# Kernel optimization log

Hardware: AMD Instinct MI355X
Metric: run time of the kernel (lower is better)

The kernel has to match this reference:

```python
import jax, jax.numpy as jnp
import numpy as np

N = 20000      # total nodes
E = 320000     # edges before self loops
G = 64         # graphs in the batch
H = 8          # attention heads
NEG_SLOPE = 0.2
EPS = 1e-5


def _gatv2(x, src, dst, Wl, bl, Wr, br, att, bias, concat):
    # PyG GATv2Conv: xl = lin_l(x) (source/messages), xr = lin_r(x) (target)
    heads, C = att.shape
    xl = (x @ Wl + bl).reshape(-1, heads, C)
    xr = (x @ Wr + br).reshape(-1, heads, C)
    e = jax.nn.leaky_relu(xl[src] + xr[dst], NEG_SLOPE)          # [E', H, C]
    a = jnp.einsum('ehc,hc->eh', e, att)                          # [E', H]
    amax = jax.ops.segment_max(a, dst, num_segments=N)
    a = jnp.exp(a - amax[dst])
    a = a / jax.ops.segment_sum(a, dst, num_segments=N)[dst]
    out = jax.ops.segment_sum(xl[src] * a[..., None], dst, num_segments=N)
    out = out.reshape(-1, heads * C) if concat else out.mean(axis=1)
    return out + bias


def _graphnorm(x, batch, w, b, ms):
    cnt = jnp.maximum(jax.ops.segment_sum(jnp.ones((x.shape[0],), x.dtype), batch, num_segments=G), 1.0)[:, None]
    mean = jax.ops.segment_sum(x, batch, num_segments=G) / cnt
    out = x - mean[batch] * ms
    var = jax.ops.segment_sum(out * out, batch, num_segments=G) / cnt
    return w * out / jnp.sqrt(var + EPS)[batch] + b


def _mean_pool(x, batch):
    cnt = jnp.maximum(jax.ops.segment_sum(jnp.ones((x.shape[0],), x.dtype), batch, num_segments=G), 1.0)[:, None]
    return jax.ops.segment_sum(x, batch, num_segments=G) / cnt


def setup_inputs():
    key = jax.random.key(0)
    ks = iter(jax.random.split(key, 40))

    def gl(shape, scale=0.05):
        return jax.random.normal(next(ks), shape, jnp.float32) * scale

    inp = {}
    inp['x'] = jax.random.normal(next(ks), (N, 19), jnp.float32)
    inp['edge_index'] = jax.random.randint(next(ks), (2, E), 0, N, jnp.int32)
    inp['batch'] = jnp.sort(jax.random.randint(next(ks), (N,), 0, G, jnp.int32))

    # layer 1: 19 -> (8 heads x 32), concat -> 256
    inp['W1l'] = gl((19, 256)); inp['b1l'] = jnp.zeros((256,), jnp.float32)
    inp['W1r'] = gl((19, 256)); inp['b1r'] = jnp.zeros((256,), jnp.float32)
    inp['att1'] = gl((H, 32)); inp['bias1'] = jnp.zeros((256,), jnp.float32)
    inp['gn1_w'] = jnp.ones((256,), jnp.float32); inp['gn1_b'] = jnp.zeros((256,), jnp.float32); inp['gn1_ms'] = jnp.ones((256,), jnp.float32)

    inp['W2l'] = gl((256, 128)); inp['b2l'] = jnp.zeros((128,), jnp.float32)
    inp['W2r'] = gl((256, 128)); inp['b2r'] = jnp.zeros((128,), jnp.float32)
    inp['att2'] = gl((H, 16)); inp['bias2'] = jnp.zeros((128,), jnp.float32)
    inp['gn2_w'] = jnp.ones((128,), jnp.float32); inp['gn2_b'] = jnp.zeros((128,), jnp.float32); inp['gn2_ms'] = jnp.ones((128,), jnp.float32)

    inp['W3l'] = gl((128, 64)); inp['b3l'] = jnp.zeros((64,), jnp.float32)
    inp['W3r'] = gl((128, 64)); inp['b3r'] = jnp.zeros((64,), jnp.float32)
    inp['att3'] = gl((H, 8)); inp['bias3'] = jnp.zeros((8,), jnp.float32)
    inp['gn3_w'] = jnp.ones((8,), jnp.float32); inp['gn3_b'] = jnp.zeros((8,), jnp.float32); inp['gn3_ms'] = jnp.ones((8,), jnp.float32)

    inp['lin_w'] = gl((8, 4)); inp['lin_b'] = jnp.zeros((4,), jnp.float32)
    return inp


def reference(x, edge_index, batch, W1l, b1l, W1r, b1r, att1, bias1, gn1_w, gn1_b, gn1_ms,
              W2l, b2l, W2r, b2r, att2, bias2, gn2_w, gn2_b, gn2_ms,
              W3l, b3l, W3r, b3r, att3, bias3, gn3_w, gn3_b, gn3_ms, lin_w, lin_b):
    loop = jnp.arange(N, dtype=edge_index.dtype)  # GATv2Conv add_self_loops=True
    src = jnp.concatenate([edge_index[0], loop])
    dst = jnp.concatenate([edge_index[1], loop])

    h = _gatv2(x, src, dst, W1l, b1l, W1r, b1r, att1, bias1, True)
    h = jax.nn.relu(_graphnorm(h, batch, gn1_w, gn1_b, gn1_ms))
    h = _gatv2(h, src, dst, W2l, b2l, W2r, b2r, att2, bias2, True)
    h = jax.nn.relu(_graphnorm(h, batch, gn2_w, gn2_b, gn2_ms))
    h = _gatv2(h, src, dst, W3l, b3l, W3r, b3r, att3, bias3, False)
    h = jax.nn.relu(_graphnorm(h, batch, gn3_w, gn3_b, gn3_ms))

    features = _mean_pool(h, batch)        # [G, 8]
    logits = features @ lin_w + lin_b      # [G, 4]
    return (logits, features)
```

## Files before the change

kernel.cpp:

```cpp
#include <hip/hip_runtime.h>
#include <math.h>

#define NN 20000
#define EE 320000
#define GG 64
#define HH 8
#define EPSV 1e-5f

static inline unsigned int gridFor(long n, int b){ return (unsigned int)((n + b - 1)/b); }

typedef __attribute__((ext_vector_type(8))) short short8;
typedef __attribute__((ext_vector_type(4))) float f32x4;
typedef unsigned short ushort_t;

__device__ __forceinline__ float asf(unsigned int u){
    union{unsigned int i; float f;} c; c.i = u; return c.f;
}
__device__ __forceinline__ ushort_t f2bf(float x){
    unsigned u = __float_as_uint(x);
    unsigned r = u + 0x7FFFu + ((u >> 16) & 1u);
    return (ushort_t)(r >> 16);
}
__device__ __forceinline__ void split_bf16(float x, short& hi, short& lo){
    unsigned u = __float_as_uint(x);
    unsigned r = u + 0x7FFFu + ((u >> 16) & 1u);
    hi = (short)(r >> 16);
    float hf = asf(((unsigned)(unsigned short)hi) << 16);
    float res = x - hf;
    unsigned u2 = __float_as_uint(res);
    unsigned r2 = u2 + 0x7FFFu + ((u2 >> 16) & 1u);
    lo = (short)(r2 >> 16);
}

__device__ __forceinline__ void wprep_one(const float* Wl, const float* Wr,
                                          ushort_t* Whi, ushort_t* Wlo,
                                          int K, int Kp, int HC, int t){
    int octs = Kp >> 3;
    int n = t / octs, ko = t - n*octs;
    int kb = ko*8;
    const float* W = (n < HC) ? (Wl + n) : (Wr + (n - HC));
    short hi[8], lo[8];
    #pragma unroll
    for (int j = 0; j < 8; ++j){
        int k = kb + j;
        float v = (k < K) ? W[(long)k*HC] : 0.f;
        split_bf16(v, hi[j], lo[j]);
    }
    long base = (((long)(n>>4)*(Kp>>5) + (kb>>5))*64 + (n&15) + 16*((kb>>3)&3))*8;
    *(short8*)&Whi[base] = *(short8*)hi;
    *(short8*)&Wlo[base] = *(short8*)lo;
}

#define WP1 2048
#define WP2 8192
#define WP3 2048

__global__ void k_wprep_all(const float* __restrict__ W1l, const float* __restrict__ W1r,
                            const float* __restrict__ W2l, const float* __restrict__ W2r,
                            const float* __restrict__ W3l, const float* __restrict__ W3r,
                            ushort_t* __restrict__ W1hi, ushort_t* __restrict__ W1lo,
                            ushort_t* __restrict__ W2hi, ushort_t* __restrict__ W2lo,
                            ushort_t* __restrict__ W3hi, ushort_t* __restrict__ W3lo,
                            int* __restrict__ cursor){
    int t = blockIdx.x*blockDim.x + threadIdx.x;
    if (t < NN) cursor[t] = 0;
    if (t < WP1) wprep_one(W1l, W1r, W1hi, W1lo, 19, 32, 256, t);
    else if (t < WP1+WP2) wprep_one(W2l, W2r, W2hi, W2lo, 256, 256, 128, t-WP1);
    else if (t < WP1+WP2+WP3) wprep_one(W3l, W3r, W3hi, W3lo, 128, 128, 64, t-WP1-WP2);
}

__global__ void k_degbounds(const int* __restrict__ edst, int* __restrict__ deg,
                            const int* __restrict__ batch,
                            int* __restrict__ gstart, int* __restrict__ gend,
                            float* __restrict__ gz){
    int e = blockIdx.x*blockDim.x + threadIdx.x;
    if (e < EE) atomicAdd(&deg[edst[e]], 1);
    if (e < NN){
        int b = batch[e];
        if (e == 0 || batch[e-1] != b) gstart[b] = e;
        if (e == NN-1 || batch[e+1] != b) gend[b] = e+1;
    }
    if (e < 2*GG*256) gz[e] = 0.f;
}

__global__ void k_scan(int* __restrict__ deg, int* __restrict__ indptr){
    __shared__ int partial[1024];
    const int CH = (NN + 1023)/1024;
    int t = threadIdx.x;
    int base = t*CH;
    int vals[CH];
    int sum = 0;
    for (int i = 0; i < CH; ++i){
        int v = (base+i < NN) ? deg[base+i] : 0;
        vals[i] = sum; sum += v;
    }
    for (int i = 0; i < CH; ++i)
        if (base+i < NN) deg[base+i] = 0;
    partial[t] = sum;
    __syncthreads();
    for (int off = 1; off < 1024; off <<= 1){
        int v = (t >= off) ? partial[t-off] : 0;
        __syncthreads();
        partial[t] += v;
        __syncthreads();
    }
    int prefix = (t > 0) ? partial[t-1] : 0;
    for (int i = 0; i < CH; ++i)
        if (base+i < NN) indptr[base+i] = prefix + vals[i];
    if (t == 1023) indptr[NN] = prefix + sum;
}

__global__ void k_scatter(const int* __restrict__ esrc, const int* __restrict__ edst,
                          const int* __restrict__ indptr, int* __restrict__ cursor,
                          int* __restrict__ srclist){
    int e = blockIdx.x*blockDim.x + threadIdx.x;
    if (e >= EE) return;
    int d = edst[e];
    int pos = atomicAdd(&cursor[d], 1);
    srclist[indptr[d] + pos] = esrc[e];
}

template<bool NORM>
__global__ __launch_bounds__(256)
void k_gemm_mfma(const float* __restrict__ h,
                 const ushort_t* __restrict__ Whi, const ushort_t* __restrict__ Wlo,
                 const float* __restrict__ bl, const float* __restrict__ br,
                 const float* __restrict__ gmu, const float* __restrict__ ginv,
                 const float* __restrict__ nw, const float* __restrict__ nb,
                 const int* __restrict__ batch,
                 ushort_t* __restrict__ xlb, float* __restrict__ xr,
                 int K, int Kp, int HC){
    __shared__ short Ahi[2][64*32], Alo[2][64*32];
    const int tid  = threadIdx.x;
    const int lane = tid & 63;
    const int wave = tid >> 6;
    const int m0   = blockIdx.x * 64;
    const int n0   = blockIdx.y * 128;
    const int wr   = (wave & 1) * 32;
    const int wcg  = (wave >> 1) * 64;
    const int kblocks = Kp >> 5;

    const int srow = tid >> 2;
    const int soct = tid & 3;

    f32x4 acc[2][4] = {};

    for (int kb = 0; kb < kblocks; ++kb){
        int p = kb & 1;
        int k0 = kb*32;
        {
            int gm = m0 + srow;
            int kbase = k0 + soct*8;
            float v[8];
            const float* src = h + (long)gm*K + kbase;
            if (gm < NN && kbase + 8 <= K){
                float4 t0 = *(const float4*)src;
                float4 t1 = *(const float4*)(src+4);
                v[0]=t0.x; v[1]=t0.y; v[2]=t0.z; v[3]=t0.w;
                v[4]=t1.x; v[5]=t1.y; v[6]=t1.z; v[7]=t1.w;
            } else {
                #pragma unroll
                for (int j = 0; j < 8; ++j)
                    v[j] = (gm < NN && kbase + j < K) ? src[j] : 0.f;
            }
            if (NORM && gm < NN){
                int g = batch[gm];
                const float* mu = gmu + (long)g*K;
                const float* iv = ginv + (long)g*K;
                #pragma unroll
                for (int j = 0; j < 8; ++j){
                    int c = kbase + j;
                    float t = (v[j] - mu[c]) * iv[c] * nw[c] + nb[c];
                    v[j] = fmaxf(t, 0.f);
                }
            }
            short hi[8], lo[8];
            #pragma unroll
            for (int j = 0; j < 8; ++j) split_bf16(v[j], hi[j], lo[j]);
            long off = ((long)(srow>>4)*64 + (srow&15) + 16*soct)*8;
            *(short8*)&Ahi[p][off] = *(short8*)hi;
            *(short8*)&Alo[p][off] = *(short8*)lo;
        }
        __syncthreads();

        int rb0 = wr >> 4;
        short8 ah0 = *(short8*)&Ahi[p][((rb0  )*64 + lane)*8];
        short8 ah1 = *(short8*)&Ahi[p][((rb0+1)*64 + lane)*8];
        short8 al0 = *(short8*)&Alo[p][((rb0  )*64 + lane)*8];
        short8 al1 = *(short8*)&Alo[p][((rb0+1)*64 + lane)*8];

        short8 bh[4], bl_[4];
        #pragma unroll
        for (int j = 0; j < 4; ++j){
            int n = n0 + wcg + j*16;
            long bbase = (((long)(n>>4)*kblocks + kb)*64 + lane)*8;
            bh[j]  = *(const short8*)&Whi[bbase];
            bl_[j] = *(const short8*)&Wlo[bbase];
        }

        #pragma unroll
        for (int j = 0; j < 4; ++j){
            acc[0][j] = __builtin_amdgcn_mfma_f32_16x16x32_bf16(al0, bh[j],  acc[0][j], 0,0,0);
            acc[0][j] = __builtin_amdgcn_mfma_f32_16x16x32_bf16(ah0, bl_[j], acc[0][j], 0,0,0);
            acc[0][j] = __builtin_amdgcn_mfma_f32_16x16x32_bf16(ah0, bh[j],  acc[0][j], 0,0,0);
            acc[1][j] = __builtin_amdgcn_mfma_f32_16x16x32_bf16(al1, bh[j],  acc[1][j], 0,0,0);
            acc[1][j] = __builtin_amdgcn_mfma_f32_16x16x32_bf16(ah1, bl_[j], acc[1][j], 0,0,0);
            acc[1][j] = __builtin_amdgcn_mfma_f32_16x16x32_bf16(ah1, bh[j],  acc[1][j], 0,0,0);
        }
    }

    #pragma unroll
    for (int i = 0; i < 2; ++i){
        int row0 = m0 + wr + i*16 + (lane >> 4)*4;
        #pragma unroll
        for (int j = 0; j < 4; ++j){
            int n = n0 + wcg + j*16 + (lane & 15);
            float bb = (n < HC) ? bl[n] : br[n - HC];
            #pragma unroll
            for (int r = 0; r < 4; ++r){
                int gm = row0 + r;
                if (gm >= NN) continue;
                float v = acc[i][j][r] + bb;
                if (n < HC) xlb[(long)gm*HC + n] = f2bf(v);
                else        xr[(long)gm*HC + (n - HC)] = v;
            }
        }
    }
}

template<int VEC> struct VT;
template<> struct VT<1>{ using T = float;  };
template<> struct VT<2>{ using T = float2; };
template<> struct VT<4>{ using T = float4; };

template<int VEC> struct BF;
template<> struct BF<1>{
    static __device__ __forceinline__ float load(const ushort_t* p){
        return asf(((unsigned)*p) << 16);
    }
};
template<> struct BF<2>{
    static __device__ __forceinline__ float2 load(const ushort_t* p){
        unsigned u = *(const unsigned*)p;
        return make_float2(asf(u << 16), asf(u & 0xFFFF0000u));
    }
};
template<> struct BF<4>{
    static __device__ __forceinline__ float4 load(const ushort_t* p){
        uint2 u = *(const uint2*)p;
        return make_float4(asf(u.x << 16), asf(u.x & 0xFFFF0000u),
                           asf(u.y << 16), asf(u.y & 0xFFFF0000u));
    }
};

__device__ __forceinline__ float lrelu(float z){ return z > 0.f ? z : 0.2f*z; }

__device__ __forceinline__ float edot(float xv, float xr, float at){
    return lrelu(xv + xr) * at;
}
__device__ __forceinline__ float edot(float2 xv, float2 xr, float2 at){
    return lrelu(xv.x+xr.x)*at.x + lrelu(xv.y+xr.y)*at.y;
}
__device__ __forceinline__ float edot(float4 xv, float4 xr, float4 at){
    return lrelu(xv.x+xr.x)*at.x + lrelu(xv.y+xr.y)*at.y
         + lrelu(xv.z+xr.z)*at.z + lrelu(xv.w+xr.w)*at.w;
}
__device__ __forceinline__ void efma(float& o, float p, float xv){ o = fmaf(p,xv,o); }
__device__ __forceinline__ void efma(float2& o, float p, float2 xv){
    o.x = fmaf(p,xv.x,o.x); o.y = fmaf(p,xv.y,o.y);
}
__device__ __forceinline__ void efma(float4& o, float p, float4 xv){
    o.x = fmaf(p,xv.x,o.x); o.y = fmaf(p,xv.y,o.y);
    o.z = fmaf(p,xv.z,o.z); o.w = fmaf(p,xv.w,o.w);
}
__device__ __forceinline__ float escale(float o, float s, float b){ return fmaf(o,s,b); }
__device__ __forceinline__ float2 escale(float2 o, float s, float2 b){
    return make_float2(fmaf(o.x,s,b.x), fmaf(o.y,s,b.y));
}
__device__ __forceinline__ float4 escale(float4 o, float s, float4 b){
    return make_float4(fmaf(o.x,s,b.x), fmaf(o.y,s,b.y), fmaf(o.z,s,b.z), fmaf(o.w,s,b.w));
}

__device__ __forceinline__ float red8(float v){
    v += __shfl_xor(v, 1);
    v += __shfl_xor(v, 2);
    v += __shfl_xor(v, 4);
    return v;
}

template<int VEC, bool MEAN>
__global__ __launch_bounds__(256)
void k_gat_w(const int* __restrict__ indptr, const int* __restrict__ srclist,
             const ushort_t* __restrict__ xlb, const float* __restrict__ xr,
             const float* __restrict__ att, const float* __restrict__ bias,
             float* __restrict__ val){
    using V = typename VT<VEC>::T;
    constexpr int HC = 64*VEC;
    const int lane = threadIdx.x & 63;
    const int d = blockIdx.x*4 + (threadIdx.x >> 6);
    const int co = lane*VEC;

    V xrd = *(const V*)&xr[(long)d*HC + co];
    V at  = *(const V*)&att[co];
    V xls = BF<VEC>::load(xlb + (long)d*HC + co);

    float m0 = red8(edot(xls, xrd, at));
    float l = 1.0f;
    V o = xls;

    int j = indptr[d], end = indptr[d+1];
    for (; j + 8 <= end; j += 8){
        int s0 = srclist[j+0], s1 = srclist[j+1], s2 = srclist[j+2], s3 = srclist[j+3];
        int s4 = srclist[j+4], s5 = srclist[j+5], s6 = srclist[j+6], s7 = srclist[j+7];
        V x0 = BF<VEC>::load(xlb + (long)s0*HC + co);
        V x1 = BF<VEC>::load(xlb + (long)s1*HC + co);
        V x2 = BF<VEC>::load(xlb + (long)s2*HC + co);
        V x3 = BF<VEC>::load(xlb + (long)s3*HC + co);
        V x4 = BF<VEC>::load(xlb + (long)s4*HC + co);
        V x5 = BF<VEC>::load(xlb + (long)s5*HC + co);
        V x6 = BF<VEC>::load(xlb + (long)s6*HC + co);
        V x7 = BF<VEC>::load(xlb + (long)s7*HC + co);
        float a0 = red8(edot(x0, xrd, at));
        float a1 = red8(edot(x1, xrd, at));
        float a2 = red8(edot(x2, xrd, at));
        float a3 = red8(edot(x3, xrd, at));
        float a4 = red8(edot(x4, xrd, at));
        float a5 = red8(edot(x5, xrd, at));
        float a6 = red8(edot(x6, xrd, at));
        float a7 = red8(edot(x7, xrd, at));
        float p0 = __expf(a0 - m0), p1 = __expf(a1 - m0);
        float p2 = __expf(a2 - m0), p3 = __expf(a3 - m0);
        float p4 = __expf(a4 - m0), p5 = __expf(a5 - m0);
        float p6 = __expf(a6 - m0), p7 = __expf(a7 - m0);
        l += ((p0+p1)+(p2+p3)) + ((p4+p5)+(p6+p7));
        efma(o, p0, x0); efma(o, p1, x1); efma(o, p2, x2); efma(o, p3, x3);
        efma(o, p4, x4); efma(o, p5, x5); efma(o, p6, x6); efma(o, p7, x7);
    }
    for (; j < end; j += 4){
        int m = end - j;
        int s0 = srclist[j];
        int s1 = (m > 1) ? srclist[j+1] : s0;
        int s2 = (m > 2) ? srclist[j+2] : s0;
        int s3 = (m > 3) ? srclist[j+3] : s0;
        V x0 = BF<VEC>::load(xlb + (long)s0*HC + co);
        V x1 = BF<VEC>::load(xlb + (long)s1*HC + co);
        V x2 = BF<VEC>::load(xlb + (long)s2*HC + co);
        V x3 = BF<VEC>::load(xlb + (long)s3*HC + co);
        float a0 = red8(edot(x0, xrd, at));
        float a1 = red8(edot(x1, xrd, at));
        float a2 = red8(edot(x2, xrd, at));
        float a3 = red8(edot(x3, xrd, at));
        float p0 = __expf(a0 - m0);
        float p1 = __expf(a1 - m0);
        float p2 = __expf(a2 - m0);
        float p3 = __expf(a3 - m0);
        l += p0; efma(o, p0, x0);
        if (m > 1){ l += p1; efma(o, p1, x1); }
        if (m > 2){ l += p2; efma(o, p2, x2); }
        if (m > 3){ l += p3; efma(o, p3, x3); }
    }
    float invl = 1.0f / l;
    if (!MEAN){
        V bv = *(const V*)&bias[co];
        *(V*)&val[(long)d*HC + co] = escale(o, invl, bv);
    } else {
        float r = ((float&)o) * invl;
        r += __shfl_xor(r, 8);
        r += __shfl_xor(r, 16);
        r += __shfl_xor(r, 32);
        if (lane < 8) val[(long)d*8 + lane] = r*0.125f + bias[lane];
    }
}

template<int F>
__global__ void k_gn_partial(const float* __restrict__ val,
                             const int* __restrict__ gstart, const int* __restrict__ gend,
                             float* __restrict__ gsum, float* __restrict__ gsq){
    int g = blockIdx.x, ch = blockIdx.y, nch = gridDim.y;
    int c = threadIdx.x;
    int s = gstart[g], e = gend[g];
    float sum = 0.f, sq = 0.f;
    for (int i = s + ch; i < e; i += nch){
        float v = val[(long)i*F + c];
        sum += v; sq += v*v;
    }
    if (sum != 0.f || sq != 0.f){
        atomicAdd(&gsum[g*F + c], sum);
        atomicAdd(&gsq[g*F + c], sq);
    }
}

__global__ void k_gn_finalize(float* __restrict__ gsum, float* __restrict__ gsq,
                              const int* __restrict__ gstart, const int* __restrict__ gend,
                              const float* __restrict__ ms,
                              float* __restrict__ gmu, float* __restrict__ ginv, int F){
    int idx = blockIdx.x*blockDim.x + threadIdx.x;
    if (idx >= GG*F) return;
    int g = idx / F, c = idx - g*F;
    int cnti = gend[g] - gstart[g];
    float cn = cnti > 0 ? (float)cnti : 1.f;
    float mean = gsum[idx] / cn;
    float mu = mean * ms[c];
    float var = gsq[idx]/cn - 2.f*mu*mean + mu*mu;
    gmu[idx]  = mu;
    ginv[idx] = rsqrtf(var + EPSV);
    gsum[idx] = 0.f;
    gsq[idx]  = 0.f;
}

__global__ void k_tail(const float* __restrict__ D,
                       const int* __restrict__ gstart, const int* __restrict__ gend,
                       const float* __restrict__ ms, const float* __restrict__ w,
                       const float* __restrict__ b,
                       const float* __restrict__ lw, const float* __restrict__ lb,
                       float* __restrict__ outLog, float* __restrict__ outFeat){
    int g = blockIdx.x;
    int t = threadIdx.x;
    int c = t & 7, r = t >> 3;
    int s = gstart[g], e = gend[g];
    int cnti = e - s;
    float cn = cnti > 0 ? (float)cnti : 1.f;

    float sum = 0.f, sq = 0.f;
    for (int i = s + r; i < e; i += 8){
        float v = D[(long)i*8 + c];
        sum += v; sq += v*v;
    }
    #pragma unroll
    for (int mask = 8; mask < 64; mask <<= 1){
        sum += __shfl_xor(sum, mask, 64);
        sq  += __shfl_xor(sq,  mask, 64);
    }
    float mean = sum / cn;
    float mu = mean * ms[c];
    float var = sq/cn - 2.f*mu*mean + mu*mu;
    float iv = rsqrtf(var + EPSV);
    float wc = w[c], bc = b[c];

    float psum = 0.f;
    for (int i = s + r; i < e; i += 8){
        float v = (D[(long)i*8 + c] - mu) * iv * wc + bc;
        psum += fmaxf(v, 0.f);
    }
    #pragma unroll
    for (int mask = 8; mask < 64; mask <<= 1)
        psum += __shfl_xor(psum, mask, 64);
    float feat = psum / cn;

    if (t < 8) outFeat[g*8 + t] = feat;

    float a = 0.f;
    int jj = t;
    if (t < 4){
        a = lb[jj];
    }
    #pragma unroll
    for (int cc = 0; cc < 8; ++cc){
        float fc = __shfl(feat, cc, 64);
        if (t < 4) a += fc * lw[cc*4 + jj];
    }
    if (t < 4) outLog[g*4 + jj] = a;
}

extern "C" void kernel_launch(void* const* d_in, const int* in_sizes, int n_in,
                              void* d_out, int out_size, void* d_ws, size_t ws_size,
                              hipStream_t stream) {
    const float* x     = (const float*)d_in[0];
    const int*   ei    = (const int*)  d_in[1];
    const int*   batch = (const int*)  d_in[2];
    const float* W1l = (const float*)d_in[3];  const float* b1l = (const float*)d_in[4];
    const float* W1r = (const float*)d_in[5];  const float* b1r = (const float*)d_in[6];
    const float* att1= (const float*)d_in[7];  const float* bias1=(const float*)d_in[8];
    const float* g1w = (const float*)d_in[9];  const float* g1b = (const float*)d_in[10];
    const float* g1m = (const float*)d_in[11];
    const float* W2l = (const float*)d_in[12]; const float* b2l = (const float*)d_in[13];
    const float* W2r = (const float*)d_in[14]; const float* b2r = (const float*)d_in[15];
    const float* att2= (const float*)d_in[16]; const float* bias2=(const float*)d_in[17];
    const float* g2w = (const float*)d_in[18]; const float* g2b = (const float*)d_in[19];
    const float* g2m = (const float*)d_in[20];
    const float* W3l = (const float*)d_in[21]; const float* b3l = (const float*)d_in[22];
    const float* W3r = (const float*)d_in[23]; const float* b3r = (const float*)d_in[24];
    const float* att3= (const float*)d_in[25]; const float* bias3=(const float*)d_in[26];
    const float* g3w = (const float*)d_in[27]; const float* g3b = (const float*)d_in[28];
    const float* g3m = (const float*)d_in[29];
    const float* lin_w=(const float*)d_in[30]; const float* lin_b=(const float*)d_in[31];

    const int* esrc = ei;
    const int* edst = ei + EE;

    float* ws = (float*)d_ws;
    int*   cursor  = (int*)(ws + 0);
    int*   indptr  = (int*)(ws + 20480);
    int*   srclist = (int*)(ws + 40960);
    int*   gstart  = (int*)(ws + 361472);
    int*   gend    = (int*)(ws + 361984);
    float* gmu     = ws + 362496;
    float* ginv    = ws + 378880;
    float* gsumP   = ws + 395264;
    float* gsqP    = ws + 411648;
    ushort_t* W1hi = (ushort_t*)(ws + 428032);
    ushort_t* W1lo = (ushort_t*)(ws + 436224);
    ushort_t* W2hi = (ushort_t*)(ws + 444416);
    ushort_t* W2lo = (ushort_t*)(ws + 477184);
    ushort_t* W3hi = (ushort_t*)(ws + 509952);
    ushort_t* W3lo = (ushort_t*)(ws + 518144);
    ushort_t* Bb = (ushort_t*)(ws + 526336);
    float* Cb = ws + 3086336;
    float* D  = ws + 8206336;

    const int TB = 256;
    const int MBm = (NN + 63)/64;
    const int NCH = 32;

    k_wprep_all<<<gridFor(NN, TB), TB, 0, stream>>>(W1l, W1r, W2l, W2r, W3l, W3r,
        W1hi, W1lo, W2hi, W2lo, W3hi, W3lo, cursor);
    k_degbounds<<<gridFor(EE, TB), TB, 0, stream>>>(edst, cursor, batch, gstart, gend, gsumP);
    k_scan<<<1, 1024, 0, stream>>>(cursor, indptr);
    k_scatter<<<gridFor(EE, TB), TB, 0, stream>>>(esrc, edst, indptr, cursor, srclist);

    k_gemm_mfma<false><<<dim3(MBm, 4), 256, 0, stream>>>(x, W1hi, W1lo, b1l, b1r,
        nullptr, nullptr, nullptr, nullptr, nullptr, Bb, Cb, 19, 32, 256);
    k_gat_w<4, false><<<NN/4, 256, 0, stream>>>(indptr, srclist, Bb, Cb, att1, bias1, D);
    k_gn_partial<256><<<dim3(GG, NCH), 256, 0, stream>>>(D, gstart, gend, gsumP, gsqP);
    k_gn_finalize<<<gridFor(GG*256, TB), TB, 0, stream>>>(gsumP, gsqP, gstart, gend, g1m, gmu, ginv, 256);

    k_gemm_mfma<true><<<dim3(MBm, 2), 256, 0, stream>>>(D, W2hi, W2lo, b2l, b2r,
        gmu, ginv, g1w, g1b, batch, Bb, Cb, 256, 256, 128);
    k_gat_w<2, false><<<NN/4, 256, 0, stream>>>(indptr, srclist, Bb, Cb, att2, bias2, D);
    k_gn_partial<128><<<dim3(GG, NCH), 128, 0, stream>>>(D, gstart, gend, gsumP, gsqP);
    k_gn_finalize<<<gridFor(GG*128, TB), TB, 0, stream>>>(gsumP, gsqP, gstart, gend, g2m, gmu, ginv, 128);

    k_gemm_mfma<true><<<dim3(MBm, 1), 256, 0, stream>>>(D, W3hi, W3lo, b3l, b3r,
        gmu, ginv, g2w, g2b, batch, Bb, Cb, 128, 128, 64);
    k_gat_w<1, true><<<NN/4, 256, 0, stream>>>(indptr, srclist, Bb, Cb, att3, bias3, D);

    float* outLog  = (float*)d_out;
    float* outFeat = outLog + GG*4;
    k_tail<<<GG, 64, 0, stream>>>(D, gstart, gend, g3m, g3w, g3b, lin_w, lin_b, outLog, outFeat);
}
```

Measured before the change: 344.7 us.

## Split GAT aggregation across channel blocks, fuse scatter with first GEMM, vectorize scan

The layer-1 and layer-2 attention aggregation kernels now use one scalar channel per lane and split the channels over a second grid dimension. This gives more waves per destination node and uses narrower per-lane loads, but each slice re-reads the neighbour list. The edge-scatter CSR build is merged into the first GEMM launch as extra blocks, which removes one launch and lets the two run concurrently. The scan kernel loads and stores in int4 chunks, relying on NN being 1000*20.

```diff
diff --git a/kernel.cpp b/kernel.cpp
--- a/kernel.cpp
+++ b/kernel.cpp
@@ -85,17 +85,22 @@
 
 __global__ void k_scan(int* __restrict__ deg, int* __restrict__ indptr){
     __shared__ int partial[1024];
-    const int CH = (NN + 1023)/1024;
     int t = threadIdx.x;
-    int base = t*CH;
-    int vals[CH];
+    int vals[20];
     int sum = 0;
-    for (int i = 0; i < CH; ++i){
-        int v = (base+i < NN) ? deg[base+i] : 0;
-        vals[i] = sum; sum += v;
-    }
-    for (int i = 0; i < CH; ++i)
-        if (base+i < NN) deg[base+i] = 0;
+    if (t < 1000){
+        int4 buf[5];
+        const int4* p = (const int4*)(deg + t*20);
+        #pragma unroll
+        for (int i = 0; i < 5; ++i) buf[i] = p[i];
+        const int* bv = (const int*)buf;
+        #pragma unroll
+        for (int i = 0; i < 20; ++i){ vals[i] = sum; sum += bv[i]; }
+        int4 z = make_int4(0,0,0,0);
+        int4* pz = (int4*)(deg + t*20);
+        #pragma unroll
+        for (int i = 0; i < 5; ++i) pz[i] = z;
+    }
     partial[t] = sum;
     __syncthreads();
     for (int off = 1; off < 1024; off <<= 1){
@@ -105,37 +110,33 @@
         __syncthreads();
     }
     int prefix = (t > 0) ? partial[t-1] : 0;
-    for (int i = 0; i < CH; ++i)
-        if (base+i < NN) indptr[base+i] = prefix + vals[i];
-    if (t == 1023) indptr[NN] = prefix + sum;
-}
-
-__global__ void k_scatter(const int* __restrict__ esrc, const int* __restrict__ edst,
-                          const int* __restrict__ indptr, int* __restrict__ cursor,
-                          int* __restrict__ srclist){
-    int e = blockIdx.x*blockDim.x + threadIdx.x;
-    if (e >= EE) return;
-    int d = edst[e];
-    int pos = atomicAdd(&cursor[d], 1);
-    srclist[indptr[d] + pos] = esrc[e];
+    if (t < 1000){
+        int out[20];
+        #pragma unroll
+        for (int i = 0; i < 20; ++i) out[i] = prefix + vals[i];
+        int4* q = (int4*)(indptr + t*20);
+        #pragma unroll
+        for (int i = 0; i < 5; ++i) q[i] = ((const int4*)out)[i];
+    }
+    if (t == 1023) indptr[NN] = prefix;
 }
 
 template<bool NORM>
-__global__ __launch_bounds__(256)
-void k_gemm_mfma(const float* __restrict__ h,
-                 const ushort_t* __restrict__ Whi, const ushort_t* __restrict__ Wlo,
-                 const float* __restrict__ bl, const float* __restrict__ br,
-                 const float* __restrict__ gmu, const float* __restrict__ ginv,
-                 const float* __restrict__ nw, const float* __restrict__ nb,
-                 const int* __restrict__ batch,
-                 ushort_t* __restrict__ xlb, float* __restrict__ xr,
-                 int K, int Kp, int HC){
+__device__ __forceinline__ void gemm_body(
+    const float* __restrict__ h,
+    const ushort_t* __restrict__ Whi, const ushort_t* __restrict__ Wlo,
+    const float* __restrict__ bl, const float* __restrict__ br,
+    const float* __restrict__ gmu, const float* __restrict__ ginv,
+    const float* __restrict__ nw, const float* __restrict__ nb,
+    const int* __restrict__ batch,
+    ushort_t* __restrict__ xlb, float* __restrict__ xr,
+    int K, int Kp, int HC, int bm, int bn){
     __shared__ short Ahi[2][64*32], Alo[2][64*32];
     const int tid  = threadIdx.x;
     const int lane = tid & 63;
     const int wave = tid >> 6;
-    const int m0   = blockIdx.x * 64;
-    const int n0   = blockIdx.y * 128;
+    const int m0   = bm * 64;
+    const int n0   = bn * 128;
     const int wr   = (wave & 1) * 32;
     const int wcg  = (wave >> 1) * 64;
     const int kblocks = Kp >> 5;
@@ -228,113 +229,97 @@
     }
 }
 
-template<int VEC> struct VT;
-template<> struct VT<1>{ using T = float;  };
-template<> struct VT<2>{ using T = float2; };
-template<> struct VT<4>{ using T = float4; };
-
-template<int VEC> struct BF;
-template<> struct BF<1>{
-    static __device__ __forceinline__ float load(const ushort_t* p){
-        return asf(((unsigned)*p) << 16);
-    }
-};
-template<> struct BF<2>{
-    static __device__ __forceinline__ float2 load(const ushort_t* p){
-        unsigned u = *(const unsigned*)p;
-        return make_float2(asf(u << 16), asf(u & 0xFFFF0000u));
-    }
-};
-template<> struct BF<4>{
-    static __device__ __forceinline__ float4 load(const ushort_t* p){
-        uint2 u = *(const uint2*)p;
-        return make_float4(asf(u.x << 16), asf(u.x & 0xFFFF0000u),
-                           asf(u.y << 16), asf(u.y & 0xFFFF0000u));
-    }
-};
+template<bool NORM>
+__global__ __launch_bounds__(256)
+void k_gemm_mfma(const float* __restrict__ h,
+                 const ushort_t* __restrict__ Whi, const ushort_t* __restrict__ Wlo,
+                 const float* __restrict__ bl, const float* __restrict__ br,
+                 const float* __restrict__ gmu, const float* __restrict__ ginv,
+                 const float* __restrict__ nw, const float* __restrict__ nb,
+                 const int* __restrict__ batch,
+                 ushort_t* __restrict__ xlb, float* __restrict__ xr,
+                 int K, int Kp, int HC){
+    gemm_body<NORM>(h, Whi, Wlo, bl, br, gmu, ginv, nw, nb, batch, xlb, xr,
+                    K, Kp, HC, blockIdx.x, blockIdx.y);
+}
+
+__global__ __launch_bounds__(256)
+void k_gemm1_scatter(const float* __restrict__ x,
+                     const ushort_t* __restrict__ Whi, const ushort_t* __restrict__ Wlo,
+                     const float* __restrict__ bl, const float* __restrict__ br,
+                     ushort_t* __restrict__ xlb, float* __restrict__ xr,
+                     const int* __restrict__ esrc, const int* __restrict__ edst,
+                     const int* __restrict__ indptr, int* __restrict__ cursor,
+                     int* __restrict__ srclist, int nGemm, int mb){
+    if ((int)blockIdx.x < nGemm){
+        gemm_body<false>(x, Whi, Wlo, bl, br, nullptr, nullptr, nullptr, nullptr,
+                         nullptr, xlb, xr, 19, 32, 256, blockIdx.x % mb, blockIdx.x / mb);
+    } else {
+        int e = (blockIdx.x - nGemm)*256 + threadIdx.x;
+        if (e < EE){
+            int d = edst[e];
+            int pos = atomicAdd(&cursor[d], 1);
+            srclist[indptr[d] + pos] = esrc[e];
+        }
+    }
+}
 
 __device__ __forceinline__ float lrelu(float z){ return z > 0.f ? z : 0.2f*z; }
 
-__device__ __forceinline__ float edot(float xv, float xr, float at){
-    return lrelu(xv + xr) * at;
-}
-__device__ __forceinline__ float edot(float2 xv, float2 xr, float2 at){
-    return lrelu(xv.x+xr.x)*at.x + lrelu(xv.y+xr.y)*at.y;
-}
-__device__ __forceinline__ float edot(float4 xv, float4 xr, float4 at){
-    return lrelu(xv.x+xr.x)*at.x + lrelu(xv.y+xr.y)*at.y
-         + lrelu(xv.z+xr.z)*at.z + lrelu(xv.w+xr.w)*at.w;
-}
-__device__ __forceinline__ void efma(float& o, float p, float xv){ o = fmaf(p,xv,o); }
-__device__ __forceinline__ void efma(float2& o, float p, float2 xv){
-    o.x = fmaf(p,xv.x,o.x); o.y = fmaf(p,xv.y,o.y);
-}
-__device__ __forceinline__ void efma(float4& o, float p, float4 xv){
-    o.x = fmaf(p,xv.x,o.x); o.y = fmaf(p,xv.y,o.y);
-    o.z = fmaf(p,xv.z,o.z); o.w = fmaf(p,xv.w,o.w);
-}
-__device__ __forceinline__ float escale(float o, float s, float b){ return fmaf(o,s,b); }
-__device__ __forceinline__ float2 escale(float2 o, float s, float2 b){
-    return make_float2(fmaf(o.x,s,b.x), fmaf(o.y,s,b.y));
-}
-__device__ __forceinline__ float4 escale(float4 o, float s, float4 b){
-    return make_float4(fmaf(o.x,s,b.x), fmaf(o.y,s,b.y), fmaf(o.z,s,b.z), fmaf(o.w,s,b.w));
-}
-
-__device__ __forceinline__ float red8(float v){
-    v += __shfl_xor(v, 1);
-    v += __shfl_xor(v, 2);
-    v += __shfl_xor(v, 4);
+template<int C>
+__device__ __forceinline__ float redC(float v){
+    #pragma unroll
+    for (int m = 1; m < C; m <<= 1) v += __shfl_xor(v, m);
     return v;
 }
-
-template<int VEC, bool MEAN>
+__device__ __forceinline__ float bfld(const ushort_t* p){
+    return asf(((unsigned)*p) << 16);
+}
+
+template<int C>
 __global__ __launch_bounds__(256)
-void k_gat_w(const int* __restrict__ indptr, const int* __restrict__ srclist,
+void k_gat_s(const int* __restrict__ indptr, const int* __restrict__ srclist,
              const ushort_t* __restrict__ xlb, const float* __restrict__ xr,
              const float* __restrict__ att, const float* __restrict__ bias,
-             float* __restrict__ val){
-    using V = typename VT<VEC>::T;
-    constexpr int HC = 64*VEC;
+             float* __restrict__ val, int HC){
     const int lane = threadIdx.x & 63;
     const int d = blockIdx.x*4 + (threadIdx.x >> 6);
-    const int co = lane*VEC;
-
-    V xrd = *(const V*)&xr[(long)d*HC + co];
-    V at  = *(const V*)&att[co];
-    V xls = BF<VEC>::load(xlb + (long)d*HC + co);
-
-    float m0 = red8(edot(xls, xrd, at));
-    float l = 1.0f;
-    V o = xls;
+    const int co = blockIdx.y*64 + lane;
+    const long rowd = (long)d*HC + co;
+
+    const float xrd = xr[rowd];
+    const float at  = att[co];
+    float xls = bfld(xlb + rowd);
+    float m0 = redC<C>(lrelu(xls + xrd) * at);
+    float l = 1.f, o = xls;
 
     int j = indptr[d], end = indptr[d+1];
     for (; j + 8 <= end; j += 8){
         int s0 = srclist[j+0], s1 = srclist[j+1], s2 = srclist[j+2], s3 = srclist[j+3];
         int s4 = srclist[j+4], s5 = srclist[j+5], s6 = srclist[j+6], s7 = srclist[j+7];
-        V x0 = BF<VEC>::load(xlb + (long)s0*HC + co);
-        V x1 = BF<VEC>::load(xlb + (long)s1*HC + co);
-        V x2 = BF<VEC>::load(xlb + (long)s2*HC + co);
-        V x3 = BF<VEC>::load(xlb + (long)s3*HC + co);
-        V x4 = BF<VEC>::load(xlb + (long)s4*HC + co);
-        V x5 = BF<VEC>::load(xlb + (long)s5*HC + co);
-        V x6 = BF<VEC>::load(xlb + (long)s6*HC + co);
-        V x7 = BF<VEC>::load(xlb + (long)s7*HC + co);
-        float a0 = red8(edot(x0, xrd, at));
-        float a1 = red8(edot(x1, xrd, at));
-        float a2 = red8(edot(x2, xrd, at));
-        float a3 = red8(edot(x3, xrd, at));
-        float a4 = red8(edot(x4, xrd, at));
-        float a5 = red8(edot(x5, xrd, at));
-        float a6 = red8(edot(x6, xrd, at));
-        float a7 = red8(edot(x7, xrd, at));
+        float x0 = bfld(xlb + (long)s0*HC + co);
+        float x1 = bfld(xlb + (long)s1*HC + co);
+        float x2 = bfld(xlb + (long)s2*HC + co);
+        float x3 = bfld(xlb + (long)s3*HC + co);
+        float x4 = bfld(xlb + (long)s4*HC + co);
+        float x5 = bfld(xlb + (long)s5*HC + co);
+        float x6 = bfld(xlb + (long)s6*HC + co);
+        float x7 = bfld(xlb + (long)s7*HC + co);
+        float a0 = redC<C>(lrelu(x0 + xrd) * at);
+        float a1 = redC<C>(lrelu(x1 + xrd) * at);
+        float a2 = redC<C>(lrelu(x2 + xrd) * at);
+        float a3 = redC<C>(lrelu(x3 + xrd) * at);
+        float a4 = redC<C>(lrelu(x4 + xrd) * at);
+        float a5 = redC<C>(lrelu(x5 + xrd) * at);
+        float a6 = redC<C>(lrelu(x6 + xrd) * at);
+        float a7 = redC<C>(lrelu(x7 + xrd) * at);
         float p0 = __expf(a0 - m0), p1 = __expf(a1 - m0);
         float p2 = __expf(a2 - m0), p3 = __expf(a3 - m0);
         float p4 = __expf(a4 - m0), p5 = __expf(a5 - m0);
         float p6 = __expf(a6 - m0), p7 = __expf(a7 - m0);
         l += ((p0+p1)+(p2+p3)) + ((p4+p5)+(p6+p7));
-        efma(o, p0, x0); efma(o, p1, x1); efma(o, p2, x2); efma(o, p3, x3);
-        efma(o, p4, x4); efma(o, p5, x5); efma(o, p6, x6); efma(o, p7, x7);
+        o = fmaf(p0,x0,o); o = fmaf(p1,x1,o); o = fmaf(p2,x2,o); o = fmaf(p3,x3,o);
+        o = fmaf(p4,x4,o); o = fmaf(p5,x5,o); o = fmaf(p6,x6,o); o = fmaf(p7,x7,o);
     }
     for (; j < end; j += 4){
         int m = end - j;
@@ -342,34 +327,98 @@
         int s1 = (m > 1) ? srclist[j+1] : s0;
         int s2 = (m > 2) ? srclist[j+2] : s0;
         int s3 = (m > 3) ? srclist[j+3] : s0;
-        V x0 = BF<VEC>::load(xlb + (long)s0*HC + co);
-        V x1 = BF<VEC>::load(xlb + (long)s1*HC + co);
-        V x2 = BF<VEC>::load(xlb + (long)s2*HC + co);
-        V x3 = BF<VEC>::load(xlb + (long)s3*HC + co);
-        float a0 = red8(edot(x0, xrd, at));
-        float a1 = red8(edot(x1, xrd, at));
-        float a2 = red8(edot(x2, xrd, at));
-        float a3 = red8(edot(x3, xrd, at));
+        float x0 = bfld(xlb + (long)s0*HC + co);
+        float x1 = bfld(xlb + (long)s1*HC + co);
+        float x2 = bfld(xlb + (long)s2*HC + co);
+        float x3 = bfld(xlb + (long)s3*HC + co);
+        float a0 = redC<C>(lrelu(x0 + xrd) * at);
+        float a1 = redC<C>(lrelu(x1 + xrd) * at);
+        float a2 = redC<C>(lrelu(x2 + xrd) * at);
+        float a3 = redC<C>(lrelu(x3 + xrd) * at);
         float p0 = __expf(a0 - m0);
         float p1 = __expf(a1 - m0);
         float p2 = __expf(a2 - m0);
         float p3 = __expf(a3 - m0);
-        l += p0; efma(o, p0, x0);
-        if (m > 1){ l += p1; efma(o, p1, x1); }
-        if (m > 2){ l += p2; efma(o, p2, x2); }
-        if (m > 3){ l += p3; efma(o, p3, x3); }
-    }
-    float invl = 1.0f / l;
-    if (!MEAN){
-        V bv = *(const V*)&bias[co];
-        *(V*)&val[(long)d*HC + co] = escale(o, invl, bv);
-    } else {
-        float r = ((float&)o) * invl;
-        r += __shfl_xor(r, 8);
-        r += __shfl_xor(r, 16);
-        r += __shfl_xor(r, 32);
-        if (lane < 8) val[(long)d*8 + lane] = r*0.125f + bias[lane];
-    }
+        l += p0; o = fmaf(p0,x0,o);
+        if (m > 1){ l += p1; o = fmaf(p1,x1,o); }
+        if (m > 2){ l += p2; o = fmaf(p2,x2,o); }
+        if (m > 3){ l += p3; o = fmaf(p3,x3,o); }
+    }
+    val[rowd] = o * (1.0f/l) + bias[co];
+}
+
+__global__ __launch_bounds__(256)
+void k_gat3(const int* __restrict__ indptr, const int* __restrict__ srclist,
+            const ushort_t* __restrict__ xlb, const float* __restrict__ xr,
+            const float* __restrict__ att, const float* __restrict__ bias,
+            float* __restrict__ val){
+    const int HC = 64;
+    const int lane = threadIdx.x & 63;
+    const int d = blockIdx.x*4 + (threadIdx.x >> 6);
+    const long rowd = (long)d*HC + lane;
+
+    const float xrd = xr[rowd];
+    const float at  = att[lane];
+    float xls = bfld(xlb + rowd);
+    float m0 = redC<8>(lrelu(xls + xrd) * at);
+    float l = 1.f, o = xls;
+
+    int j = indptr[d], end = indptr[d+1];
+    for (; j + 8 <= end; j += 8){
+        int s0 = srclist[j+0], s1 = srclist[j+1], s2 = srclist[j+2], s3 = srclist[j+3];
+        int s4 = srclist[j+4], s5 = srclist[j+5], s6 = srclist[j+6], s7 = srclist[j+7];
+        float x0 = bfld(xlb + (long)s0*HC + lane);
+        float x1 = bfld(xlb + (long)s1*HC + lane);
+        float x2 = bfld(xlb + (long)s2*HC + lane);
+        float x3 = bfld(xlb + (long)s3*HC + lane);
+        float x4 = bfld(xlb + (long)s4*HC + lane);
+        float x5 = bfld(xlb + (long)s5*HC + lane);
+        float x6 = bfld(xlb + (long)s6*HC + lane);
+        float x7 = bfld(xlb + (long)s7*HC + lane);
+        float a0 = redC<8>(lrelu(x0 + xrd) * at);
+        float a1 = redC<8>(lrelu(x1 + xrd) * at);
+        float a2 = redC<8>(lrelu(x2 + xrd) * at);
+        float a3 = redC<8>(lrelu(x3 + xrd) * at);
+        float a4 = redC<8>(lrelu(x4 + xrd) * at);
+        float a5 = redC<8>(lrelu(x5 + xrd) * at);
+        float a6 = redC<8>(lrelu(x6 + xrd) * at);
+        float a7 = redC<8>(lrelu(x7 + xrd) * at);
+        float p0 = __expf(a0 - m0), p1 = __expf(a1 - m0);
+        float p2 = __expf(a2 - m0), p3 = __expf(a3 - m0);
+        float p4 = __expf(a4 - m0), p5 = __expf(a5 - m0);
+        float p6 = __expf(a6 - m0), p7 = __expf(a7 - m0);
+        l += ((p0+p1)+(p2+p3)) + ((p4+p5)+(p6+p7));
+        o = fmaf(p0,x0,o); o = fmaf(p1,x1,o); o = fmaf(p2,x2,o); o = fmaf(p3,x3,o);
+        o = fmaf(p4,x4,o); o = fmaf(p5,x5,o); o = fmaf(p6,x6,o); o = fmaf(p7,x7,o);
+    }
+    for (; j < end; j += 4){
+        int m = end - j;
+        int s0 = srclist[j];
+        int s1 = (m > 1) ? srclist[j+1] : s0;
+        int s2 = (m > 2) ? srclist[j+2] : s0;
+        int s3 = (m > 3) ? srclist[j+3] : s0;
+        float x0 = bfld(xlb + (long)s0*HC + lane);
+        float x1 = bfld(xlb + (long)s1*HC + lane);
+        float x2 = bfld(xlb + (long)s2*HC + lane);
+        float x3 = bfld(xlb + (long)s3*HC + lane);
+        float a0 = redC<8>(lrelu(x0 + xrd) * at);
+        float a1 = redC<8>(lrelu(x1 + xrd) * at);
+        float a2 = redC<8>(lrelu(x2 + xrd) * at);
+        float a3 = redC<8>(lrelu(x3 + xrd) * at);
+        float p0 = __expf(a0 - m0);
+        float p1 = __expf(a1 - m0);
+        float p2 = __expf(a2 - m0);
+        float p3 = __expf(a3 - m0);
+        l += p0; o = fmaf(p0,x0,o);
+        if (m > 1){ l += p1; o = fmaf(p1,x1,o); }
+        if (m > 2){ l += p2; o = fmaf(p2,x2,o); }
+        if (m > 3){ l += p3; o = fmaf(p3,x3,o); }
+    }
+    float r = o * (1.0f/l);
+    r += __shfl_xor(r, 8);
+    r += __shfl_xor(r, 16);
+    r += __shfl_xor(r, 32);
+    if (lane < 8) val[(long)d*8 + lane] = r*0.125f + bias[lane];
 }
 
 template<int F>
@@ -451,9 +500,7 @@
 
     float a = 0.f;
     int jj = t;
-    if (t < 4){
-        a = lb[jj];
-    }
+    if (t < 4) a = lb[jj];
     #pragma unroll
     for (int cc = 0; cc < 8; ++cc){
         float fc = __shfl(feat, cc, 64);
@@ -516,23 +563,26 @@
         W1hi, W1lo, W2hi, W2lo, W3hi, W3lo, cursor);
     k_degbounds<<<gridFor(EE, TB), TB, 0, stream>>>(edst, cursor, batch, gstart, gend, gsumP);
     k_scan<<<1, 1024, 0, stream>>>(cursor, indptr);
-    k_scatter<<<gridFor(EE, TB), TB, 0, stream>>>(esrc, edst, indptr, cursor, srclist);
-
-    k_gemm_mfma<false><<<dim3(MBm, 4), 256, 0, stream>>>(x, W1hi, W1lo, b1l, b1r,
-        nullptr, nullptr, nullptr, nullptr, nullptr, Bb, Cb, 19, 32, 256);
-    k_gat_w<4, false><<<NN/4, 256, 0, stream>>>(indptr, srclist, Bb, Cb, att1, bias1, D);
+    {
+        int nGemm = MBm*4;
+        int nScat = gridFor(EE, TB);
+        k_gemm1_scatter<<<nGemm + nScat, 256, 0, stream>>>(x, W1hi, W1lo, b1l, b1r,
+            Bb, Cb, esrc, edst, indptr, cursor, srclist, nGemm, MBm);
+    }
+
+    k_gat_s<32><<<dim3(NN/4, 4), 256, 0, stream>>>(indptr, srclist, Bb, Cb, att1, bias1, D, 256);
     k_gn_partial<256><<<dim3(GG, NCH), 256, 0, stream>>>(D, gstart, gend, gsumP, gsqP);
     k_gn_finalize<<<gridFor(GG*256, TB), TB, 0, stream>>>(gsumP, gsqP, gstart, gend, g1m, gmu, ginv, 256);
 
     k_gemm_mfma<true><<<dim3(MBm, 2), 256, 0, stream>>>(D, W2hi, W2lo, b2l, b2r,
         gmu, ginv, g1w, g1b, batch, Bb, Cb, 256, 256, 128);
-    k_gat_w<2, false><<<NN/4, 256, 0, stream>>>(indptr, srclist, Bb, Cb, att2, bias2, D);
+    k_gat_s<16><<<dim3(NN/4, 2), 256, 0, stream>>>(indptr, srclist, Bb, Cb, att2, bias2, D, 128);
     k_gn_partial<128><<<dim3(GG, NCH), 128, 0, stream>>>(D, gstart, gend, gsumP, gsqP);
     k_gn_finalize<<<gridFor(GG*128, TB), TB, 0, stream>>>(gsumP, gsqP, gstart, gend, g2m, gmu, ginv, 128);
 
     k_gemm_mfma<true><<<dim3(MBm, 1), 256, 0, stream>>>(D, W3hi, W3lo, b3l, b3r,
         gmu, ginv, g2w, g2b, batch, Bb, Cb, 128, 128, 64);
-    k_gat_w<1, true><<<NN/4, 256, 0, stream>>>(indptr, srclist, Bb, Cb, att3, bias3, D);
+    k_gat3<<<NN/4, 256, 0, stream>>>(indptr, srclist, Bb, Cb, att3, bias3, D);
 
     float* outLog  = (float*)d_out;
     float* outFeat = outLog + GG*4;
```

Result: slower. 384.0 us (+11.4%).

## Fuse layer-1 GEMM with CSR scatter launch and vectorize scan

Applied to the files above, without the earlier changes.

Merges the first-layer projection GEMM and the edge scatter into one launch, with each block branching on its index to run either a GEMM tile or a scatter chunk, so the two independent jobs run concurrently and one launch is removed. The single-block scan now has each of 1000 threads handle exactly 20 entries using int4 loads and stores instead of scalar accesses. This relies on NN being exactly 20000 and 16-byte alignment of deg and indptr. The fused kernel carries the GEMM's shared memory and register budget into the scatter blocks, which may limit how many scatter blocks fit on a compute unit at once.

```diff
diff --git a/kernel.cpp b/kernel.cpp
--- a/kernel.cpp
+++ b/kernel.cpp
@@ -85,17 +85,22 @@
 
 __global__ void k_scan(int* __restrict__ deg, int* __restrict__ indptr){
     __shared__ int partial[1024];
-    const int CH = (NN + 1023)/1024;
     int t = threadIdx.x;
-    int base = t*CH;
-    int vals[CH];
+    int vals[20];
     int sum = 0;
-    for (int i = 0; i < CH; ++i){
-        int v = (base+i < NN) ? deg[base+i] : 0;
-        vals[i] = sum; sum += v;
-    }
-    for (int i = 0; i < CH; ++i)
-        if (base+i < NN) deg[base+i] = 0;
+    if (t < 1000){
+        int4 buf[5];
+        const int4* p = (const int4*)(deg + t*20);
+        #pragma unroll
+        for (int i = 0; i < 5; ++i) buf[i] = p[i];
+        const int* bv = (const int*)buf;
+        #pragma unroll
+        for (int i = 0; i < 20; ++i){ vals[i] = sum; sum += bv[i]; }
+        int4 z = make_int4(0,0,0,0);
+        int4* pz = (int4*)(deg + t*20);
+        #pragma unroll
+        for (int i = 0; i < 5; ++i) pz[i] = z;
+    }
     partial[t] = sum;
     __syncthreads();
     for (int off = 1; off < 1024; off <<= 1){
@@ -105,37 +110,33 @@
         __syncthreads();
     }
     int prefix = (t > 0) ? partial[t-1] : 0;
-    for (int i = 0; i < CH; ++i)
-        if (base+i < NN) indptr[base+i] = prefix + vals[i];
-    if (t == 1023) indptr[NN] = prefix + sum;
-}
-
-__global__ void k_scatter(const int* __restrict__ esrc, const int* __restrict__ edst,
-                          const int* __restrict__ indptr, int* __restrict__ cursor,
-                          int* __restrict__ srclist){
-    int e = blockIdx.x*blockDim.x + threadIdx.x;
-    if (e >= EE) return;
-    int d = edst[e];
-    int pos = atomicAdd(&cursor[d], 1);
-    srclist[indptr[d] + pos] = esrc[e];
+    if (t < 1000){
+        int out[20];
+        #pragma unroll
+        for (int i = 0; i < 20; ++i) out[i] = prefix + vals[i];
+        int4* q = (int4*)(indptr + t*20);
+        #pragma unroll
+        for (int i = 0; i < 5; ++i) q[i] = ((const int4*)out)[i];
+    }
+    if (t == 1023) indptr[NN] = prefix;
 }
 
 template<bool NORM>
-__global__ __launch_bounds__(256)
-void k_gemm_mfma(const float* __restrict__ h,
-                 const ushort_t* __restrict__ Whi, const ushort_t* __restrict__ Wlo,
-                 const float* __restrict__ bl, const float* __restrict__ br,
-                 const float* __restrict__ gmu, const float* __restrict__ ginv,
-                 const float* __restrict__ nw, const float* __restrict__ nb,
-                 const int* __restrict__ batch,
-                 ushort_t* __restrict__ xlb, float* __restrict__ xr,
-                 int K, int Kp, int HC){
+__device__ __forceinline__ void gemm_body(
+    const float* __restrict__ h,
+    const ushort_t* __restrict__ Whi, const ushort_t* __restrict__ Wlo,
+    const float* __restrict__ bl, const float* __restrict__ br,
+    const float* __restrict__ gmu, const float* __restrict__ ginv,
+    const float* __restrict__ nw, const float* __restrict__ nb,
+    const int* __restrict__ batch,
+    ushort_t* __restrict__ xlb, float* __restrict__ xr,
+    int K, int Kp, int HC, int bm, int bn){
     __shared__ short Ahi[2][64*32], Alo[2][64*32];
     const int tid  = threadIdx.x;
     const int lane = tid & 63;
     const int wave = tid >> 6;
-    const int m0   = blockIdx.x * 64;
-    const int n0   = blockIdx.y * 128;
+    const int m0   = bm * 64;
+    const int n0   = bn * 128;
     const int wr   = (wave & 1) * 32;
     const int wcg  = (wave >> 1) * 64;
     const int kblocks = Kp >> 5;
@@ -228,6 +229,41 @@
     }
 }
 
+template<bool NORM>
+__global__ __launch_bounds__(256)
+void k_gemm_mfma(const float* __restrict__ h,
+                 const ushort_t* __restrict__ Whi, const ushort_t* __restrict__ Wlo,
+                 const float* __restrict__ bl, const float* __restrict__ br,
+                 const float* __restrict__ gmu, const float* __restrict__ ginv,
+                 const float* __restrict__ nw, const float* __restrict__ nb,
+                 const int* __restrict__ batch,
+                 ushort_t* __restrict__ xlb, float* __restrict__ xr,
+                 int K, int Kp, int HC){
+    gemm_body<NORM>(h, Whi, Wlo, bl, br, gmu, ginv, nw, nb, batch, xlb, xr,
+                    K, Kp, HC, blockIdx.x, blockIdx.y);
+}
+
+__global__ __launch_bounds__(256)
+void k_gemm1_scatter(const float* __restrict__ x,
+                     const ushort_t* __restrict__ Whi, const ushort_t* __restrict__ Wlo,
+                     const float* __restrict__ bl, const float* __restrict__ br,
+                     ushort_t* __restrict__ xlb, float* __restrict__ xr,
+                     const int* __restrict__ esrc, const int* __restrict__ edst,
+                     const int* __restrict__ indptr, int* __restrict__ cursor,
+                     int* __restrict__ srclist, int nGemm, int mb){
+    if ((int)blockIdx.x < nGemm){
+        gemm_body<false>(x, Whi, Wlo, bl, br, nullptr, nullptr, nullptr, nullptr,
+                         nullptr, xlb, xr, 19, 32, 256, blockIdx.x % mb, blockIdx.x / mb);
+    } else {
+        int e = (blockIdx.x - nGemm)*256 + threadIdx.x;
+        if (e < EE){
+            int d = edst[e];
+            int pos = atomicAdd(&cursor[d], 1);
+            srclist[indptr[d] + pos] = esrc[e];
+        }
+    }
+}
+
 template<int VEC> struct VT;
 template<> struct VT<1>{ using T = float;  };
 template<> struct VT<2>{ using T = float2; };
@@ -451,9 +487,7 @@
 
     float a = 0.f;
     int jj = t;
-    if (t < 4){
-        a = lb[jj];
-    }
+    if (t < 4) a = lb[jj];
     #pragma unroll
     for (int cc = 0; cc < 8; ++cc){
         float fc = __shfl(feat, cc, 64);
@@ -516,10 +550,13 @@
         W1hi, W1lo, W2hi, W2lo, W3hi, W3lo, cursor);
     k_degbounds<<<gridFor(EE, TB), TB, 0, stream>>>(edst, cursor, batch, gstart, gend, gsumP);
     k_scan<<<1, 1024, 0, stream>>>(cursor, indptr);
-    k_scatter<<<gridFor(EE, TB), TB, 0, stream>>>(esrc, edst, indptr, cursor, srclist);
-
-    k_gemm_mfma<false><<<dim3(MBm, 4), 256, 0, stream>>>(x, W1hi, W1lo, b1l, b1r,
-        nullptr, nullptr, nullptr, nullptr, nullptr, Bb, Cb, 19, 32, 256);
+    {
+        int nGemm = MBm*4;
+        int nScat = gridFor(EE, TB);
+        k_gemm1_scatter<<<nGemm + nScat, 256, 0, stream>>>(x, W1hi, W1lo, b1l, b1r,
+            Bb, Cb, esrc, edst, indptr, cursor, srclist, nGemm, MBm);
+    }
+
     k_gat_w<4, false><<<NN/4, 256, 0, stream>>>(indptr, srclist, Bb, Cb, att1, bias1, D);
     k_gn_partial<256><<<dim3(GG, NCH), 256, 0, stream>>>(D, gstart, gend, gsumP, gsqP);
     k_gn_finalize<<<gridFor(GG*256, TB), TB, 0, stream>>>(gsumP, gsqP, gstart, gend, g1m, gmu, ginv, 256);
```

Result: faster. 324.3 us (-5.9%).
